# Performance work log

Measured on AMD Instinct MI355X. Metric: run time of the kernel, lower is better.

## Reference

```python
import jax, jax.numpy as jnp
import numpy as np
import math

D_MODEL, N_HEADS, D_K, D_V = 512, 2, 64, 64
C_CLIP = 10.0
MASK_FILL = -10.0

def setup_inputs() -> dict:
    key = jax.random.key(0)
    ks = jax.random.split(key, 12)
    B, Lq, Lk = 4, 2048, 2048
    s = 1.0 / math.sqrt(D_MODEL)
    return {
        "Q": jax.random.normal(ks[0], (B, Lq, D_MODEL), jnp.float32),
        "K": jax.random.normal(ks[1], (B, Lk, D_MODEL), jnp.float32),
        "V": jax.random.normal(ks[2], (B, Lk, D_MODEL), jnp.float32),
        "mask": jax.random.randint(ks[3], (B, Lk), 0, 2) > 0,
        "Wq": jax.random.normal(ks[4], (D_MODEL, N_HEADS * D_K), jnp.float32) * s,
        "bq": jnp.zeros((N_HEADS * D_K,), jnp.float32),
        "Wk": jax.random.normal(ks[5], (D_MODEL, N_HEADS * D_K), jnp.float32) * s,
        "bk": jnp.zeros((N_HEADS * D_K,), jnp.float32),
        "Wv": jax.random.normal(ks[6], (D_MODEL, N_HEADS * D_V), jnp.float32) * s,
        "bv": jnp.zeros((N_HEADS * D_V,), jnp.float32),
        "Wo": jax.random.normal(ks[7], (N_HEADS * D_V, D_MODEL), jnp.float32) * s,
        "bo": jnp.zeros((D_MODEL,), jnp.float32),
    }

def reference(Q, K, V, mask, Wq, bq, Wk, bk, Wv, bv, Wo, bo):
    B, Lq, _ = Q.shape
    Lk = K.shape[1]
    # project and split heads: [B, h, L, d]
    q = (Q @ Wq + bq).reshape(B, Lq, N_HEADS, D_K).transpose(0, 2, 1, 3)
    k = (K @ Wk + bk).reshape(B, Lk, N_HEADS, D_K).transpose(0, 2, 1, 3)
    v = (V @ Wv + bv).reshape(B, Lk, N_HEADS, D_V).transpose(0, 2, 1, 3)
    scores = jnp.einsum("bhqd,bhkd->bhqk", q, k) / jnp.sqrt(jnp.float32(D_K))
    scores = jnp.tanh(scores) * C_CLIP
    scores = jnp.where(mask[:, None, None, :], MASK_FILL, scores)
    attn = jax.nn.log_softmax(scores, axis=-1)  # NOTE: log-softmax used directly as weights
    out = jnp.einsum("bhqk,bhkd->bhqd", attn, v)
    out = out.transpose(0, 2, 1, 3).reshape(B, Lq, N_HEADS * D_V)
    out = out @ Wo + bo
    return (out, attn)
```

## Files before the change

### kernel.cpp

```cpp
#include <hip/hip_runtime.h>

typedef __attribute__((ext_vector_type(8))) short short8;
typedef __attribute__((ext_vector_type(4))) short short4v;
typedef __attribute__((ext_vector_type(4))) float f32x4;

#define DEVI static __device__ __forceinline__

constexpr int NB   = 4;
constexpr int NH   = 2;
constexpr int SEQ  = 2048;
constexpr int DM   = 512;
constexpr int DKV  = 64;
constexpr int HDIM = 128;

DEVI unsigned short f2bf(float f) {
    union { float f; unsigned u; } v; v.f = f;
    unsigned r = v.u + 0x7FFFu + ((v.u >> 16) & 1u);
    return (unsigned short)(r >> 16);
}
DEVI float bf2f(unsigned short s) {
    union { unsigned u; float f; } v; v.u = ((unsigned)s) << 16; return v.f;
}
DEVI void async16(const void* g, void* l) {
    __builtin_amdgcn_global_load_lds(
        (const __attribute__((address_space(1))) unsigned int*)g,
        (__attribute__((address_space(3))) unsigned int*)l, 16, 0, 0);
}

__global__ __launch_bounds__(256) void k_prep(
    const float* __restrict__ Wq, const float* __restrict__ Wk,
    const float* __restrict__ Wv, const float* __restrict__ Wo,
    unsigned short* __restrict__ Wqt, unsigned short* __restrict__ Wkt,
    unsigned short* __restrict__ Wvt, unsigned short* __restrict__ Wot) {
    int id = blockIdx.x * 256 + threadIdx.x;
    int which = id >> 16;
    int rem = id & 65535;
    if (which < 3) {
        const float* W = which == 0 ? Wq : (which == 1 ? Wk : Wv);
        unsigned short* Wt = which == 0 ? Wqt : (which == 1 ? Wkt : Wvt);
        int n = rem >> 9, k = rem & 511;
        Wt[rem] = f2bf(W[k * HDIM + n]);
    } else {
        int n = rem >> 7, k = rem & 127;
        Wot[rem] = f2bf(Wo[k * DM + n]);
    }
}

__global__ __launch_bounds__(256) void k_proj(
    const float* __restrict__ Qg, const float* __restrict__ Kg, const float* __restrict__ Vg,
    const unsigned short* __restrict__ Wqt, const unsigned short* __restrict__ Wkt,
    const unsigned short* __restrict__ Wvt,
    const float* __restrict__ bq, const float* __restrict__ bk, const float* __restrict__ bv,
    unsigned short* __restrict__ qs, unsigned short* __restrict__ kb,
    unsigned short* __restrict__ vt) {
    __shared__ unsigned short lA[64 * 64];
    __shared__ unsigned short lB[128 * 64];

    const int y = blockIdx.y;
    const float* X = y == 0 ? Qg : (y == 1 ? Kg : Vg);
    const unsigned short* Wt = y == 0 ? Wqt : (y == 1 ? Wkt : Wvt);
    const float* bias = y == 0 ? bq : (y == 1 ? bk : bv);
    const float scal = y == 0 ? 0.125f : 1.0f;
    const int row0 = blockIdx.x * 64;
    const int tid = threadIdx.x, lane = tid & 63, wv = tid >> 6;
    const int l16 = lane & 15, lq4 = lane >> 4;
    const int wr = wv >> 1, wc = wv & 1;

    f32x4 acc[2][4];
    #pragma unroll
    for (int i = 0; i < 2; ++i)
        #pragma unroll
        for (int j = 0; j < 4; ++j) acc[i][j] = f32x4{0.f, 0.f, 0.f, 0.f};

    const int arow = tid >> 2, ac0 = (tid & 3) * 16;

    for (int kc = 0; kc < 8; ++kc) {
        {
            const float* src = X + (size_t)(row0 + arow) * DM + kc * 64 + ac0;
            unsigned short* dst = &lA[arow * 64 + ac0];
            #pragma unroll
            for (int i = 0; i < 4; ++i) {
                float4 v = *(const float4*)(src + 4 * i);
                unsigned p0 = (unsigned)f2bf(v.x) | ((unsigned)f2bf(v.y) << 16);
                unsigned p1 = (unsigned)f2bf(v.z) | ((unsigned)f2bf(v.w) << 16);
                *(unsigned*)(dst + 4 * i) = p0;
                *(unsigned*)(dst + 4 * i + 2) = p1;
            }
        }
        #pragma unroll
        for (int c = 0; c < 4; ++c) {
            int chunk = wv * 4 + c;
            int n = chunk * 8 + (lane >> 3);
            int kpart = (lane & 7) * 8;
            const void* g = (const char*)Wt + ((size_t)n * DM + kc * 64 + kpart) * 2;
            void* l = (char*)lB + chunk * 1024 + lane * 16;
            async16(g, l);
        }
        __syncthreads();

        #pragma unroll
        for (int ks = 0; ks < 2; ++ks) {
            short8 a[2], b[4];
            #pragma unroll
            for (int mt = 0; mt < 2; ++mt) {
                int m = wr * 32 + mt * 16 + l16;
                a[mt] = *(const short8*)&lA[m * 64 + ks * 32 + lq4 * 8];
            }
            #pragma unroll
            for (int nt = 0; nt < 4; ++nt) {
                int n = wc * 64 + nt * 16 + l16;
                b[nt] = *(const short8*)&lB[n * 64 + ks * 32 + lq4 * 8];
            }
            #pragma unroll
            for (int mt = 0; mt < 2; ++mt)
                #pragma unroll
                for (int nt = 0; nt < 4; ++nt)
                    acc[mt][nt] = __builtin_amdgcn_mfma_f32_16x16x32_bf16(
                        a[mt], b[nt], acc[mt][nt], 0, 0, 0);
        }
        __syncthreads();
    }

    if (y < 2) {
        unsigned short* dstp = (y == 0) ? qs : kb;
        #pragma unroll
        for (int mt = 0; mt < 2; ++mt)
            #pragma unroll
            for (int nt = 0; nt < 4; ++nt) {
                int col = wc * 64 + nt * 16 + l16;
                float bb = bias[col];
                int h = col >> 6, d = col & 63;
                #pragma unroll
                for (int r = 0; r < 4; ++r) {
                    int row = row0 + wr * 32 + mt * 16 + lq4 * 4 + r;
                    int b = row >> 11, pos = row & 2047;
                    float val = (acc[mt][nt][r] + bb) * scal;
                    dstp[((size_t)(b * NH + h) * SEQ + pos) * DKV + d] = f2bf(val);
                }
            }
    } else {
        #pragma unroll
        for (int mt = 0; mt < 2; ++mt)
            #pragma unroll
            for (int nt = 0; nt < 4; ++nt) {
                int col = wc * 64 + nt * 16 + l16;
                float bb = bias[col];
                #pragma unroll
                for (int r = 0; r < 4; ++r) {
                    int mrow = wr * 32 + mt * 16 + lq4 * 4 + r;
                    lB[col * 64 + mrow] = f2bf(acc[mt][nt][r] + bb);
                }
            }
        __syncthreads();
        int c = tid >> 1, mp = (tid & 1) * 32;
        int b = row0 >> 11, kpos0 = row0 & 2047;
        int h = c >> 6, d = c & 63;
        unsigned short* dst = vt + ((size_t)(b * NH + h) * DKV + d) * SEQ + kpos0 + mp;
        const unsigned short* srcl = &lB[c * 64 + mp];
        #pragma unroll
        for (int i = 0; i < 4; ++i)
            *(uint4*)(dst + 8 * i) = *(const uint4*)(srcl + 8 * i);
    }
}

__global__ __launch_bounds__(256) void k_pass1(
    const unsigned short* __restrict__ qs, const unsigned short* __restrict__ kb,
    const int* __restrict__ maskg, float* __restrict__ Lpart) {
    __shared__ unsigned short lK[128 * 64];
    __shared__ int lM[128];
    __shared__ float lsumW[4 * 64];

    const int bx = blockIdx.x;
    const int ksp = bx & 3;
    const int qt = (bx >> 2) & 31;
    const int bh = bx >> 7;
    const int qbase = qt * 64;
    const int b = bh >> 1;
    const int tid = threadIdx.x, lane = tid & 63, wv = tid >> 6;
    const int l16 = lane & 15, lq4 = lane >> 4;

    short8 aq[4][2];
    #pragma unroll
    for (int mt = 0; mt < 4; ++mt)
        #pragma unroll
        for (int ks = 0; ks < 2; ++ks) {
            size_t off = ((size_t)bh * SEQ + qbase + mt * 16 + l16) * DKV + ks * 32 + lq4 * 8;
            aq[mt][ks] = *(const short8*)(qs + off);
        }

    float sums[4][4];
    #pragma unroll
    for (int mt = 0; mt < 4; ++mt)
        #pragma unroll
        for (int r = 0; r < 4; ++r) sums[mt][r] = 0.f;

    const char* kbase_ptr = (const char*)(kb + (size_t)bh * SEQ * DKV);

    for (int kt = ksp * 4; kt < ksp * 4 + 4; ++kt) {
        int kbase = kt * 128;
        #pragma unroll
        for (int c = 0; c < 4; ++c) {
            int chunk = wv * 4 + c;
            const void* g = kbase_ptr + (size_t)kbase * 128 + chunk * 1024 + lane * 16;
            void* l = (char*)lK + chunk * 1024 + lane * 16;
            async16(g, l);
        }
        if (tid < 128) lM[tid] = maskg[b * SEQ + kbase + tid];
        __syncthreads();

        f32x4 acc[4][2];
        #pragma unroll
        for (int mt = 0; mt < 4; ++mt)
            #pragma unroll
            for (int nt = 0; nt < 2; ++nt) acc[mt][nt] = f32x4{0.f, 0.f, 0.f, 0.f};
        #pragma unroll
        for (int ks = 0; ks < 2; ++ks) {
            short8 bfr[2];
            #pragma unroll
            for (int nt = 0; nt < 2; ++nt) {
                int n = wv * 32 + nt * 16 + l16;
                bfr[nt] = *(const short8*)&lK[n * 64 + ks * 32 + lq4 * 8];
            }
            #pragma unroll
            for (int mt = 0; mt < 4; ++mt)
                #pragma unroll
                for (int nt = 0; nt < 2; ++nt)
                    acc[mt][nt] = __builtin_amdgcn_mfma_f32_16x16x32_bf16(
                        aq[mt][ks], bfr[nt], acc[mt][nt], 0, 0, 0);
        }
        #pragma unroll
        for (int nt = 0; nt < 2; ++nt) {
            int col = wv * 32 + nt * 16 + l16;
            int mv = lM[col];
            #pragma unroll
            for (int mt = 0; mt < 4; ++mt)
                #pragma unroll
                for (int r = 0; r < 4; ++r) {
                    float x = acc[mt][nt][r];
                    float e2 = __expf(2.f * x);
                    float s10 = 10.f - 20.f * __builtin_amdgcn_rcpf(1.f + e2);
                    float s = mv ? -10.f : s10;
                    sums[mt][r] += __expf(s);
                }
        }
        __syncthreads();
    }

    #pragma unroll
    for (int mt = 0; mt < 4; ++mt)
        #pragma unroll
        for (int r = 0; r < 4; ++r) {
            float v = sums[mt][r];
            v += __shfl_xor(v, 1); v += __shfl_xor(v, 2);
            v += __shfl_xor(v, 4); v += __shfl_xor(v, 8);
            if (l16 == 0) lsumW[wv * 64 + mt * 16 + lq4 * 4 + r] = v;
        }
    __syncthreads();
    if (tid < 64) {
        float v = lsumW[tid] + lsumW[64 + tid] + lsumW[128 + tid] + lsumW[192 + tid];
        Lpart[(size_t)ksp * (8 * SEQ) + (size_t)bh * SEQ + qbase + tid] = v;
    }
}

__global__ __launch_bounds__(256) void k_pass2(
    const unsigned short* __restrict__ qs, const unsigned short* __restrict__ kb,
    const unsigned short* __restrict__ vt, const int* __restrict__ maskg,
    const float* __restrict__ Lpart, float* __restrict__ attnG, float* __restrict__ outh2) {
    __shared__ unsigned short lK[128 * 64];
    __shared__ unsigned short lV[64 * 128];
    __shared__ unsigned short lAttn[64 * 136];
    __shared__ int lM[128];

    const int bx = blockIdx.x;
    const int ksp = bx & 3;
    const int qt = (bx >> 2) & 31;
    const int bh = bx >> 7;
    const int qbase = qt * 64;
    const int b = bh >> 1, h = bh & 1;
    const int tid = threadIdx.x, lane = tid & 63, wv = tid >> 6;
    const int l16 = lane & 15, lq4 = lane >> 4;

    short8 aq[4][2];
    #pragma unroll
    for (int mt = 0; mt < 4; ++mt)
        #pragma unroll
        for (int ks = 0; ks < 2; ++ks) {
            size_t off = ((size_t)bh * SEQ + qbase + mt * 16 + l16) * DKV + ks * 32 + lq4 * 8;
            aq[mt][ks] = *(const short8*)(qs + off);
        }

    float Lr[4][4];
    #pragma unroll
    for (int mt = 0; mt < 4; ++mt)
        #pragma unroll
        for (int r = 0; r < 4; ++r) {
            size_t idx = (size_t)bh * SEQ + qbase + mt * 16 + lq4 * 4 + r;
            float s = Lpart[idx] + Lpart[8 * SEQ + idx] +
                      Lpart[2 * 8 * SEQ + idx] + Lpart[3 * 8 * SEQ + idx];
            Lr[mt][r] = __logf(s);
        }

    f32x4 o[4];
    #pragma unroll
    for (int mt = 0; mt < 4; ++mt) o[mt] = f32x4{0.f, 0.f, 0.f, 0.f};

    const char* kbase_ptr = (const char*)(kb + (size_t)bh * SEQ * DKV);

    for (int kt = ksp * 4; kt < ksp * 4 + 4; ++kt) {
        int kbase = kt * 128;
        #pragma unroll
        for (int c = 0; c < 4; ++c) {
            int chunk = wv * 4 + c;
            const void* g = kbase_ptr + (size_t)kbase * 128 + chunk * 1024 + lane * 16;
            void* l = (char*)lK + chunk * 1024 + lane * 16;
            async16(g, l);
        }
        #pragma unroll
        for (int c = 0; c < 4; ++c) {
            int chunk = wv * 4 + c;
            int d = chunk * 4 + (lane >> 4);
            int kk = (lane & 15) * 8;
            const void* g = (const char*)vt + (((size_t)bh * DKV + d) * SEQ + kbase + kk) * 2;
            void* l = (char*)lV + chunk * 1024 + lane * 16;
            async16(g, l);
        }
        if (tid < 128) lM[tid] = maskg[b * SEQ + kbase + tid];
        __syncthreads();

        f32x4 s[4][2];
        #pragma unroll
        for (int mt = 0; mt < 4; ++mt)
            #pragma unroll
            for (int nt = 0; nt < 2; ++nt) s[mt][nt] = f32x4{0.f, 0.f, 0.f, 0.f};
        #pragma unroll
        for (int ks = 0; ks < 2; ++ks) {
            short8 bfr[2];
            #pragma unroll
            for (int nt = 0; nt < 2; ++nt) {
                int n = wv * 32 + nt * 16 + l16;
                bfr[nt] = *(const short8*)&lK[n * 64 + ks * 32 + lq4 * 8];
            }
            #pragma unroll
            for (int mt = 0; mt < 4; ++mt)
                #pragma unroll
                for (int nt = 0; nt < 2; ++nt)
                    s[mt][nt] = __builtin_amdgcn_mfma_f32_16x16x32_bf16(
                        aq[mt][ks], bfr[nt], s[mt][nt], 0, 0, 0);
        }
        #pragma unroll
        for (int nt = 0; nt < 2; ++nt) {
            int col = wv * 32 + nt * 16 + l16;
            int mv = lM[col];
            #pragma unroll
            for (int mt = 0; mt < 4; ++mt)
                #pragma unroll
                for (int r = 0; r < 4; ++r) {
                    float x = s[mt][nt][r];
                    float e2 = __expf(2.f * x);
                    float s10 = 10.f - 20.f * __builtin_amdgcn_rcpf(1.f + e2);
                    float a = (mv ? -10.f : s10) - Lr[mt][r];
                    lAttn[(mt * 16 + lq4 * 4 + r) * 136 + col] = f2bf(a);
                }
        }
        __syncthreads();

        #pragma unroll
        for (int ks = 0; ks < 4; ++ks) {
            short8 bfr = *(const short8*)&lV[(wv * 16 + l16) * 128 + ks * 32 + lq4 * 8];
            #pragma unroll
            for (int mt = 0; mt < 4; ++mt) {
                short8 af = *(const short8*)&lAttn[(mt * 16 + l16) * 136 + ks * 32 + lq4 * 8];
                o[mt] = __builtin_amdgcn_mfma_f32_16x16x32_bf16(af, bfr, o[mt], 0, 0, 0);
            }
        }
        #pragma unroll
        for (int j = 0; j < 8; ++j) {
            int row = j * 8 + (tid >> 5);
            int col = (tid & 31) * 4;
            short4v hv = *(const short4v*)&lAttn[row * 136 + col];
            float4 f;
            f.x = bf2f((unsigned short)hv[0]); f.y = bf2f((unsigned short)hv[1]);
            f.z = bf2f((unsigned short)hv[2]); f.w = bf2f((unsigned short)hv[3]);
            float* gdst = attnG + ((size_t)bh * SEQ + qbase + row) * SEQ + kbase + col;
            *(float4*)gdst = f;
        }
        __syncthreads();
    }

    float* dst = outh2 + (size_t)ksp * (8192 * HDIM);
    #pragma unroll
    for (int mt = 0; mt < 4; ++mt)
        #pragma unroll
        for (int r = 0; r < 4; ++r) {
            int q = qbase + mt * 16 + lq4 * 4 + r;
            int dcol = wv * 16 + l16;
            dst[((size_t)b * SEQ + q) * HDIM + h * DKV + dcol] = o[mt][r];
        }
}

__global__ __launch_bounds__(256) void k_comb(const float* __restrict__ outh2,
                                              unsigned short* __restrict__ outh) {
    int i = (blockIdx.x * 256 + threadIdx.x) * 4;
    float4 a = *(const float4*)(outh2 + i);
    float4 c = *(const float4*)(outh2 + 1048576 + i);
    float4 d = *(const float4*)(outh2 + 2 * 1048576 + i);
    float4 e = *(const float4*)(outh2 + 3 * 1048576 + i);
    unsigned long long pk =
        (unsigned long long)f2bf(a.x + c.x + d.x + e.x) |
        ((unsigned long long)f2bf(a.y + c.y + d.y + e.y) << 16) |
        ((unsigned long long)f2bf(a.z + c.z + d.z + e.z) << 32) |
        ((unsigned long long)f2bf(a.w + c.w + d.w + e.w) << 48);
    *(unsigned long long*)(outh + i) = pk;
}

__global__ __launch_bounds__(256) void k_oproj(
    const unsigned short* __restrict__ outh, const unsigned short* __restrict__ Wot,
    const float* __restrict__ bo, float* __restrict__ outG) {
    __shared__ unsigned short lA2[128 * 128];
    __shared__ unsigned short lB2[128 * 128];
    const int row0 = blockIdx.x * 128, col0 = blockIdx.y * 128;
    const int tid = threadIdx.x, lane = tid & 63, wv = tid >> 6;
    const int l16 = lane & 15, lq4 = lane >> 4;
    const int wr = wv >> 1, wc = wv & 1;

    #pragma unroll
    for (int c = 0; c < 8; ++c) {
        int chunk = wv * 8 + c;
        const void* g = (const char*)outh + (size_t)row0 * 256 + chunk * 1024 + lane * 16;
        void* l = (char*)lA2 + chunk * 1024 + lane * 16;
        async16(g, l);
    }
    #pragma unroll
    for (int c = 0; c < 8; ++c) {
        int chunk = wv * 8 + c;
        const void* g = (const char*)Wot + (size_t)col0 * 256 + chunk * 1024 + lane * 16;
        void* l = (char*)lB2 + chunk * 1024 + lane * 16;
        async16(g, l);
    }
    __syncthreads();

    f32x4 acc[4][4];
    #pragma unroll
    for (int mt = 0; mt < 4; ++mt)
        #pragma unroll
        for (int nt = 0; nt < 4; ++nt) acc[mt][nt] = f32x4{0.f, 0.f, 0.f, 0.f};

    #pragma unroll
    for (int ks = 0; ks < 4; ++ks) {
        short8 a[4], bfr[4];
        #pragma unroll
        for (int mt = 0; mt < 4; ++mt)
            a[mt] = *(const short8*)&lA2[(wr * 64 + mt * 16 + l16) * 128 + ks * 32 + lq4 * 8];
        #pragma unroll
        for (int nt = 0; nt < 4; ++nt)
            bfr[nt] = *(const short8*)&lB2[(wc * 64 + nt * 16 + l16) * 128 + ks * 32 + lq4 * 8];
        #pragma unroll
        for (int mt = 0; mt < 4; ++mt)
            #pragma unroll
            for (int nt = 0; nt < 4; ++nt)
                acc[mt][nt] = __builtin_amdgcn_mfma_f32_16x16x32_bf16(
                    a[mt], bfr[nt], acc[mt][nt], 0, 0, 0);
    }

    #pragma unroll
    for (int nt = 0; nt < 4; ++nt) {
        int col = col0 + wc * 64 + nt * 16 + l16;
        float bb = bo[col];
        #pragma unroll
        for (int mt = 0; mt < 4; ++mt)
            #pragma unroll
            for (int r = 0; r < 4; ++r) {
                int row = row0 + wr * 64 + mt * 16 + lq4 * 4 + r;
                outG[(size_t)row * DM + col] = acc[mt][nt][r] + bb;
            }
    }
}

extern "C" void kernel_launch(void* const* d_in, const int* in_sizes, int n_in,
                              void* d_out, int out_size, void* d_ws, size_t ws_size,
                              hipStream_t stream) {
    (void)in_sizes; (void)n_in; (void)out_size; (void)ws_size;
    const float* Qg = (const float*)d_in[0];
    const float* Kg = (const float*)d_in[1];
    const float* Vg = (const float*)d_in[2];
    const int*   maskg = (const int*)d_in[3];
    const float* Wq = (const float*)d_in[4];
    const float* bq = (const float*)d_in[5];
    const float* Wk = (const float*)d_in[6];
    const float* bk = (const float*)d_in[7];
    const float* Wv = (const float*)d_in[8];
    const float* bv = (const float*)d_in[9];
    const float* Wo = (const float*)d_in[10];
    const float* bo = (const float*)d_in[11];

    char* ws = (char*)d_ws;
    unsigned short* qs   = (unsigned short*)(ws);
    unsigned short* kb   = (unsigned short*)(ws + (4  << 20));
    unsigned short* vt   = (unsigned short*)(ws + (8  << 20));
    float*          outh2= (float*)(ws + (12 << 20));
    unsigned short* outh = (unsigned short*)(ws + (28 << 20));
    float*          Lpart= (float*)(ws + (30 << 20));
    unsigned short* Wqt  = (unsigned short*)(ws + (30 << 20) + 262144);
    unsigned short* Wkt  = (unsigned short*)((char*)Wqt + 131072);
    unsigned short* Wvt  = (unsigned short*)((char*)Wkt + 131072);
    unsigned short* Wot  = (unsigned short*)((char*)Wvt + 131072);

    float* outG  = (float*)d_out;
    float* attnG = outG + (size_t)NB * SEQ * DM;

    hipLaunchKernelGGL(k_prep, dim3(1024), dim3(256), 0, stream,
                       Wq, Wk, Wv, Wo, Wqt, Wkt, Wvt, Wot);
    hipLaunchKernelGGL(k_proj, dim3(128, 3), dim3(256), 0, stream,
                       Qg, Kg, Vg, Wqt, Wkt, Wvt, bq, bk, bv, qs, kb, vt);
    hipLaunchKernelGGL(k_pass1, dim3(1024), dim3(256), 0, stream, qs, kb, maskg, Lpart);
    hipLaunchKernelGGL(k_pass2, dim3(1024), dim3(256), 0, stream,
                       qs, kb, vt, maskg, Lpart, attnG, outh2);
    hipLaunchKernelGGL(k_comb, dim3(1024), dim3(256), 0, stream, outh2, outh);
    hipLaunchKernelGGL(k_oproj, dim3(64, 4), dim3(256), 0, stream, outh, Wot, bo, outG);
}
```

Baseline: 261.7 us.

## Store clipped scores in pass1, factor log-sum out of PV, fuse combine

Pass1 now writes the bf16 tanh-clipped scores to a 64MB workspace, so pass2 no longer recomputes QK^T. Pass2 multiplies the raw scores by V and subtracts L times the per-column sum of V, which k_proj accumulates with atomics. Pass2 also reads the stored scores to write the attention output with nontemporal stores. The combine kernel is folded into the output projection, and several shared-memory tiles get XOR swizzles or padding against bank conflicts. The cost is an extra write and read of the full score matrix through global memory, plus a small precision change from factoring out the log-sum.

```diff
diff --git a/kernel.cpp b/kernel.cpp
--- a/kernel.cpp
+++ b/kernel.cpp
@@ -1,7 +1,6 @@
 #include <hip/hip_runtime.h>
 
 typedef __attribute__((ext_vector_type(8))) short short8;
-typedef __attribute__((ext_vector_type(4))) short short4v;
 typedef __attribute__((ext_vector_type(4))) float f32x4;
 
 #define DEVI static __device__ __forceinline__
@@ -52,8 +51,8 @@
     const unsigned short* __restrict__ Wvt,
     const float* __restrict__ bq, const float* __restrict__ bk, const float* __restrict__ bv,
     unsigned short* __restrict__ qs, unsigned short* __restrict__ kb,
-    unsigned short* __restrict__ vt) {
-    __shared__ unsigned short lA[64 * 64];
+    unsigned short* __restrict__ vt, float* __restrict__ colsumv) {
+    __shared__ unsigned short lA[64 * 72];
     __shared__ unsigned short lB[128 * 64];
 
     const int y = blockIdx.y;
@@ -77,10 +76,10 @@
     for (int kc = 0; kc < 8; ++kc) {
         {
             const float* src = X + (size_t)(row0 + arow) * DM + kc * 64 + ac0;
-            unsigned short* dst = &lA[arow * 64 + ac0];
+            unsigned short* dst = &lA[arow * 72 + ac0];
             #pragma unroll
             for (int i = 0; i < 4; ++i) {
-                float4 v = *(const float4*)(src + 4 * i);
+                f32x4 v = __builtin_nontemporal_load((const f32x4*)(src + 4 * i));
                 unsigned p0 = (unsigned)f2bf(v.x) | ((unsigned)f2bf(v.y) << 16);
                 unsigned p1 = (unsigned)f2bf(v.z) | ((unsigned)f2bf(v.w) << 16);
                 *(unsigned*)(dst + 4 * i) = p0;
@@ -90,9 +89,9 @@
         #pragma unroll
         for (int c = 0; c < 4; ++c) {
             int chunk = wv * 4 + c;
-            int n = chunk * 8 + (lane >> 3);
-            int kpart = (lane & 7) * 8;
-            const void* g = (const char*)Wt + ((size_t)n * DM + kc * 64 + kpart) * 2;
+            int flat = chunk * 64 + lane;
+            int row = flat >> 3, cp = flat & 7, cc = cp ^ (row & 7);
+            const void* g = (const char*)Wt + (size_t)row * 1024 + kc * 128 + cc * 16;
             void* l = (char*)lB + chunk * 1024 + lane * 16;
             async16(g, l);
         }
@@ -104,12 +103,12 @@
             #pragma unroll
             for (int mt = 0; mt < 2; ++mt) {
                 int m = wr * 32 + mt * 16 + l16;
-                a[mt] = *(const short8*)&lA[m * 64 + ks * 32 + lq4 * 8];
+                a[mt] = *(const short8*)&lA[m * 72 + ks * 32 + lq4 * 8];
             }
             #pragma unroll
             for (int nt = 0; nt < 4; ++nt) {
                 int n = wc * 64 + nt * 16 + l16;
-                b[nt] = *(const short8*)&lB[n * 64 + ks * 32 + lq4 * 8];
+                b[nt] = *(const short8*)&lB[n * 64 + (((ks * 4 + lq4) ^ (n & 7)) * 8)];
             }
             #pragma unroll
             for (int mt = 0; mt < 2; ++mt)
@@ -152,21 +151,41 @@
                 }
             }
         __syncthreads();
-        int c = tid >> 1, mp = (tid & 1) * 32;
-        int b = row0 >> 11, kpos0 = row0 & 2047;
-        int h = c >> 6, d = c & 63;
-        unsigned short* dst = vt + ((size_t)(b * NH + h) * DKV + d) * SEQ + kpos0 + mp;
-        const unsigned short* srcl = &lB[c * 64 + mp];
-        #pragma unroll
-        for (int i = 0; i < 4; ++i)
-            *(uint4*)(dst + 8 * i) = *(const uint4*)(srcl + 8 * i);
+        {
+            int c = tid >> 1, mp = (tid & 1) * 32;
+            int b = row0 >> 11, kpos0 = row0 & 2047;
+            int h = c >> 6, d = c & 63;
+            unsigned short* dst = vt + ((size_t)(b * NH + h) * DKV + d) * SEQ + kpos0 + mp;
+            const unsigned short* srcl = &lB[c * 64 + mp];
+            #pragma unroll
+            for (int i = 0; i < 4; ++i)
+                *(uint4*)(dst + 8 * i) = *(const uint4*)(srcl + 8 * i);
+        }
+        {
+            int col = tid >> 1, half = tid & 1;
+            const unsigned short* p = &lB[col * 64 + half * 32];
+            float s = 0.f;
+            #pragma unroll
+            for (int i = 0; i < 4; ++i) {
+                short8 hv = *(const short8*)(p + 8 * i);
+                #pragma unroll
+                for (int j = 0; j < 8; ++j) s += bf2f((unsigned short)hv[j]);
+            }
+            s += __shfl_xor(s, 1);
+            if (half == 0) {
+                int ksp2 = (row0 & 2047) >> 9, bb = row0 >> 11;
+                atomicAdd(&colsumv[((size_t)ksp2 * NB + bb) * HDIM + col], s);
+            }
+        }
     }
 }
 
 __global__ __launch_bounds__(256) void k_pass1(
     const unsigned short* __restrict__ qs, const unsigned short* __restrict__ kb,
-    const int* __restrict__ maskg, float* __restrict__ Lpart) {
+    const int* __restrict__ maskg, unsigned short* __restrict__ sws,
+    float* __restrict__ Lpart) {
     __shared__ unsigned short lK[128 * 64];
+    __shared__ unsigned short lS[64 * 136];
     __shared__ int lM[128];
     __shared__ float lsumW[4 * 64];
 
@@ -201,7 +220,9 @@
         #pragma unroll
         for (int c = 0; c < 4; ++c) {
             int chunk = wv * 4 + c;
-            const void* g = kbase_ptr + (size_t)kbase * 128 + chunk * 1024 + lane * 16;
+            int flat = chunk * 64 + lane;
+            int row = flat >> 3, cp = flat & 7, cc = cp ^ (row & 7);
+            const void* g = kbase_ptr + (size_t)(kbase + row) * 128 + cc * 16;
             void* l = (char*)lK + chunk * 1024 + lane * 16;
             async16(g, l);
         }
@@ -219,7 +240,7 @@
             #pragma unroll
             for (int nt = 0; nt < 2; ++nt) {
                 int n = wv * 32 + nt * 16 + l16;
-                bfr[nt] = *(const short8*)&lK[n * 64 + ks * 32 + lq4 * 8];
+                bfr[nt] = *(const short8*)&lK[n * 64 + (((ks * 4 + lq4) ^ (n & 7)) * 8)];
             }
             #pragma unroll
             for (int mt = 0; mt < 4; ++mt)
@@ -238,12 +259,23 @@
                 for (int r = 0; r < 4; ++r) {
                     float x = acc[mt][nt][r];
                     float e2 = __expf(2.f * x);
-                    float s10 = 10.f - 20.f * __builtin_amdgcn_rcpf(1.f + e2);
-                    float s = mv ? -10.f : s10;
-                    sums[mt][r] += __expf(s);
+                    float rr = __builtin_amdgcn_rcpf(1.f + e2);
+                    rr = mv ? 1.f : rr;
+                    float s10 = __builtin_fmaf(-20.f, rr, 10.f);
+                    union { float f; unsigned u; } cv; cv.f = s10;
+                    lS[(mt * 16 + lq4 * 4 + r) * 136 + col] = (unsigned short)(cv.u >> 16);
+                    float t = __expf(-20.f * rr);
+                    sums[mt][r] = __builtin_fmaf(22026.465795f, t, sums[mt][r]);
                 }
         }
         __syncthreads();
+        #pragma unroll
+        for (int j = 0; j < 4; ++j) {
+            int row = j * 16 + (tid >> 4);
+            int coff = (tid & 15) * 8;
+            uint4 dv = *(const uint4*)&lS[row * 136 + coff];
+            *(uint4*)(sws + ((size_t)bh * SEQ + qbase + row) * SEQ + kbase + coff) = dv;
+        }
     }
 
     #pragma unroll
@@ -263,13 +295,11 @@
 }
 
 __global__ __launch_bounds__(256) void k_pass2(
-    const unsigned short* __restrict__ qs, const unsigned short* __restrict__ kb,
-    const unsigned short* __restrict__ vt, const int* __restrict__ maskg,
-    const float* __restrict__ Lpart, float* __restrict__ attnG, float* __restrict__ outh2) {
-    __shared__ unsigned short lK[128 * 64];
+    const unsigned short* __restrict__ sws, const unsigned short* __restrict__ vt,
+    const float* __restrict__ Lpart, const float* __restrict__ colsumv,
+    float* __restrict__ attnG, float* __restrict__ outh2) {
     __shared__ unsigned short lV[64 * 128];
-    __shared__ unsigned short lAttn[64 * 136];
-    __shared__ int lM[128];
+    __shared__ float lL[64];
 
     const int bx = blockIdx.x;
     const int ksp = bx & 3;
@@ -280,141 +310,84 @@
     const int tid = threadIdx.x, lane = tid & 63, wv = tid >> 6;
     const int l16 = lane & 15, lq4 = lane >> 4;
 
-    short8 aq[4][2];
+    if (tid < 64) {
+        size_t idx = (size_t)bh * SEQ + qbase + tid;
+        float s = Lpart[idx] + Lpart[8 * SEQ + idx] +
+                  Lpart[2 * 8 * SEQ + idx] + Lpart[3 * 8 * SEQ + idx];
+        lL[tid] = __logf(s);
+    }
+    __syncthreads();
+
+    float Lr[4][4];
     #pragma unroll
     for (int mt = 0; mt < 4; ++mt)
         #pragma unroll
-        for (int ks = 0; ks < 2; ++ks) {
-            size_t off = ((size_t)bh * SEQ + qbase + mt * 16 + l16) * DKV + ks * 32 + lq4 * 8;
-            aq[mt][ks] = *(const short8*)(qs + off);
-        }
-
-    float Lr[4][4];
-    #pragma unroll
-    for (int mt = 0; mt < 4; ++mt)
-        #pragma unroll
-        for (int r = 0; r < 4; ++r) {
-            size_t idx = (size_t)bh * SEQ + qbase + mt * 16 + lq4 * 4 + r;
-            float s = Lpart[idx] + Lpart[8 * SEQ + idx] +
-                      Lpart[2 * 8 * SEQ + idx] + Lpart[3 * 8 * SEQ + idx];
-            Lr[mt][r] = __logf(s);
-        }
+        for (int r = 0; r < 4; ++r) Lr[mt][r] = lL[mt * 16 + lq4 * 4 + r];
 
     f32x4 o[4];
     #pragma unroll
     for (int mt = 0; mt < 4; ++mt) o[mt] = f32x4{0.f, 0.f, 0.f, 0.f};
 
-    const char* kbase_ptr = (const char*)(kb + (size_t)bh * SEQ * DKV);
-
-    for (int kt = ksp * 4; kt < ksp * 4 + 4; ++kt) {
-        int kbase = kt * 128;
+    const unsigned short* swsb = sws + (size_t)bh * SEQ * SEQ;
+
+    for (int kti = 0; kti < 4; ++kti) {
+        int kbase = ksp * 512 + kti * 128;
         #pragma unroll
         for (int c = 0; c < 4; ++c) {
             int chunk = wv * 4 + c;
-            const void* g = kbase_ptr + (size_t)kbase * 128 + chunk * 1024 + lane * 16;
-            void* l = (char*)lK + chunk * 1024 + lane * 16;
-            async16(g, l);
-        }
-        #pragma unroll
-        for (int c = 0; c < 4; ++c) {
-            int chunk = wv * 4 + c;
-            int d = chunk * 4 + (lane >> 4);
-            int kk = (lane & 15) * 8;
-            const void* g = (const char*)vt + (((size_t)bh * DKV + d) * SEQ + kbase + kk) * 2;
+            int flat = chunk * 64 + lane;
+            int row = flat >> 4, cp = flat & 15, cc = cp ^ (row & 15);
+            const void* g = (const char*)vt +
+                (((size_t)bh * DKV + row) * SEQ + kbase) * 2 + cc * 16;
             void* l = (char*)lV + chunk * 1024 + lane * 16;
             async16(g, l);
         }
-        if (tid < 128) lM[tid] = maskg[b * SEQ + kbase + tid];
-        __syncthreads();
-
-        f32x4 s[4][2];
-        #pragma unroll
-        for (int mt = 0; mt < 4; ++mt)
-            #pragma unroll
-            for (int nt = 0; nt < 2; ++nt) s[mt][nt] = f32x4{0.f, 0.f, 0.f, 0.f};
-        #pragma unroll
-        for (int ks = 0; ks < 2; ++ks) {
-            short8 bfr[2];
-            #pragma unroll
-            for (int nt = 0; nt < 2; ++nt) {
-                int n = wv * 32 + nt * 16 + l16;
-                bfr[nt] = *(const short8*)&lK[n * 64 + ks * 32 + lq4 * 8];
-            }
-            #pragma unroll
-            for (int mt = 0; mt < 4; ++mt)
-                #pragma unroll
-                for (int nt = 0; nt < 2; ++nt)
-                    s[mt][nt] = __builtin_amdgcn_mfma_f32_16x16x32_bf16(
-                        aq[mt][ks], bfr[nt], s[mt][nt], 0, 0, 0);
-        }
-        #pragma unroll
-        for (int nt = 0; nt < 2; ++nt) {
-            int col = wv * 32 + nt * 16 + l16;
-            int mv = lM[col];
-            #pragma unroll
-            for (int mt = 0; mt < 4; ++mt)
-                #pragma unroll
-                for (int r = 0; r < 4; ++r) {
-                    float x = s[mt][nt][r];
-                    float e2 = __expf(2.f * x);
-                    float s10 = 10.f - 20.f * __builtin_amdgcn_rcpf(1.f + e2);
-                    float a = (mv ? -10.f : s10) - Lr[mt][r];
-                    lAttn[(mt * 16 + lq4 * 4 + r) * 136 + col] = f2bf(a);
-                }
-        }
         __syncthreads();
 
         #pragma unroll
         for (int ks = 0; ks < 4; ++ks) {
-            short8 bfr = *(const short8*)&lV[(wv * 16 + l16) * 128 + ks * 32 + lq4 * 8];
+            int d = wv * 16 + l16;
+            short8 bfr = *(const short8*)&lV[d * 128 + (((ks * 4 + lq4) ^ (d & 15)) * 8)];
             #pragma unroll
             for (int mt = 0; mt < 4; ++mt) {
-                short8 af = *(const short8*)&lAttn[(mt * 16 + l16) * 136 + ks * 32 + lq4 * 8];
+                const unsigned short* ap = swsb +
+                    (size_t)(qbase + mt * 16 + l16) * SEQ + kbase + ks * 32 + lq4 * 8;
+                short8 af = *(const short8*)ap;
                 o[mt] = __builtin_amdgcn_mfma_f32_16x16x32_bf16(af, bfr, o[mt], 0, 0, 0);
             }
         }
-        #pragma unroll
-        for (int j = 0; j < 8; ++j) {
-            int row = j * 8 + (tid >> 5);
-            int col = (tid & 31) * 4;
-            short4v hv = *(const short4v*)&lAttn[row * 136 + col];
-            float4 f;
-            f.x = bf2f((unsigned short)hv[0]); f.y = bf2f((unsigned short)hv[1]);
-            f.z = bf2f((unsigned short)hv[2]); f.w = bf2f((unsigned short)hv[3]);
-            float* gdst = attnG + ((size_t)bh * SEQ + qbase + row) * SEQ + kbase + col;
-            *(float4*)gdst = f;
-        }
-        __syncthreads();
-    }
-
+
+        #pragma unroll
+        for (int jr = 0; jr < 8; ++jr) {
+            int row = jr * 8 + (tid >> 5);
+            float Lv = lL[row];
+            size_t roff = (size_t)(qbase + row) * SEQ + kbase + (tid & 31) * 4;
+            uint2 w = *(const uint2*)(swsb + roff);
+            union { unsigned u; float f; } t0, t1, t2, t3;
+            t0.u = w.x << 16; t1.u = w.x & 0xFFFF0000u;
+            t2.u = w.y << 16; t3.u = w.y & 0xFFFF0000u;
+            f32x4 f;
+            f.x = t0.f - Lv; f.y = t1.f - Lv; f.z = t2.f - Lv; f.w = t3.f - Lv;
+            __builtin_nontemporal_store(f, (f32x4*)(attnG + (size_t)bh * SEQ * SEQ + roff));
+        }
+        __syncthreads();
+    }
+
+    int dcol = wv * 16 + l16;
+    float csv = colsumv[((size_t)ksp * NB + b) * HDIM + h * DKV + dcol];
     float* dst = outh2 + (size_t)ksp * (8192 * HDIM);
     #pragma unroll
     for (int mt = 0; mt < 4; ++mt)
         #pragma unroll
         for (int r = 0; r < 4; ++r) {
             int q = qbase + mt * 16 + lq4 * 4 + r;
-            int dcol = wv * 16 + l16;
-            dst[((size_t)b * SEQ + q) * HDIM + h * DKV + dcol] = o[mt][r];
-        }
-}
-
-__global__ __launch_bounds__(256) void k_comb(const float* __restrict__ outh2,
-                                              unsigned short* __restrict__ outh) {
-    int i = (blockIdx.x * 256 + threadIdx.x) * 4;
-    float4 a = *(const float4*)(outh2 + i);
-    float4 c = *(const float4*)(outh2 + 1048576 + i);
-    float4 d = *(const float4*)(outh2 + 2 * 1048576 + i);
-    float4 e = *(const float4*)(outh2 + 3 * 1048576 + i);
-    unsigned long long pk =
-        (unsigned long long)f2bf(a.x + c.x + d.x + e.x) |
-        ((unsigned long long)f2bf(a.y + c.y + d.y + e.y) << 16) |
-        ((unsigned long long)f2bf(a.z + c.z + d.z + e.z) << 32) |
-        ((unsigned long long)f2bf(a.w + c.w + d.w + e.w) << 48);
-    *(unsigned long long*)(outh + i) = pk;
+            float val = o[mt][r] - Lr[mt][r] * csv;
+            dst[((size_t)b * SEQ + q) * HDIM + h * DKV + dcol] = val;
+        }
 }
 
 __global__ __launch_bounds__(256) void k_oproj(
-    const unsigned short* __restrict__ outh, const unsigned short* __restrict__ Wot,
+    const float* __restrict__ outh2, const unsigned short* __restrict__ Wot,
     const float* __restrict__ bo, float* __restrict__ outG) {
     __shared__ unsigned short lA2[128 * 128];
     __shared__ unsigned short lB2[128 * 128];
@@ -424,16 +397,33 @@
     const int wr = wv >> 1, wc = wv & 1;
 
     #pragma unroll
+    for (int jj = 0; jj < 8; ++jj) {
+        int flat = jj * 256 + tid;
+        int row = flat >> 4, c = flat & 15;
+        size_t gr = (size_t)(row0 + row) * HDIM + c * 8;
+        float s[8];
+        #pragma unroll
+        for (int i = 0; i < 8; ++i) s[i] = 0.f;
+        #pragma unroll
+        for (int qq = 0; qq < 4; ++qq) {
+            const float4* p = (const float4*)(outh2 + (size_t)qq * 1048576 + gr);
+            float4 x0 = p[0], x1 = p[1];
+            s[0] += x0.x; s[1] += x0.y; s[2] += x0.z; s[3] += x0.w;
+            s[4] += x1.x; s[5] += x1.y; s[6] += x1.z; s[7] += x1.w;
+        }
+        unsigned d0 = (unsigned)f2bf(s[0]) | ((unsigned)f2bf(s[1]) << 16);
+        unsigned d1 = (unsigned)f2bf(s[2]) | ((unsigned)f2bf(s[3]) << 16);
+        unsigned d2 = (unsigned)f2bf(s[4]) | ((unsigned)f2bf(s[5]) << 16);
+        unsigned d3 = (unsigned)f2bf(s[6]) | ((unsigned)f2bf(s[7]) << 16);
+        uint4 pk; pk.x = d0; pk.y = d1; pk.z = d2; pk.w = d3;
+        *(uint4*)&lA2[row * 128 + ((c ^ (row & 15)) * 8)] = pk;
+    }
+    #pragma unroll
     for (int c = 0; c < 8; ++c) {
         int chunk = wv * 8 + c;
-        const void* g = (const char*)outh + (size_t)row0 * 256 + chunk * 1024 + lane * 16;
-        void* l = (char*)lA2 + chunk * 1024 + lane * 16;
-        async16(g, l);
-    }
-    #pragma unroll
-    for (int c = 0; c < 8; ++c) {
-        int chunk = wv * 8 + c;
-        const void* g = (const char*)Wot + (size_t)col0 * 256 + chunk * 1024 + lane * 16;
+        int flat = chunk * 64 + lane;
+        int row = flat >> 4, cp = flat & 15, cc = cp ^ (row & 15);
+        const void* g = (const char*)Wot + ((size_t)(col0 + row) * 128 + cc * 8) * 2;
         void* l = (char*)lB2 + chunk * 1024 + lane * 16;
         async16(g, l);
     }
@@ -449,11 +439,15 @@
     for (int ks = 0; ks < 4; ++ks) {
         short8 a[4], bfr[4];
         #pragma unroll
-        for (int mt = 0; mt < 4; ++mt)
-            a[mt] = *(const short8*)&lA2[(wr * 64 + mt * 16 + l16) * 128 + ks * 32 + lq4 * 8];
-        #pragma unroll
-        for (int nt = 0; nt < 4; ++nt)
-            bfr[nt] = *(const short8*)&lB2[(wc * 64 + nt * 16 + l16) * 128 + ks * 32 + lq4 * 8];
+        for (int mt = 0; mt < 4; ++mt) {
+            int row = wr * 64 + mt * 16 + l16;
+            a[mt] = *(const short8*)&lA2[row * 128 + (((ks * 4 + lq4) ^ (row & 15)) * 8)];
+        }
+        #pragma unroll
+        for (int nt = 0; nt < 4; ++nt) {
+            int row = wc * 64 + nt * 16 + l16;
+            bfr[nt] = *(const short8*)&lB2[row * 128 + (((ks * 4 + lq4) ^ (row & 15)) * 8)];
+        }
         #pragma unroll
         for (int mt = 0; mt < 4; ++mt)
             #pragma unroll
@@ -494,27 +488,30 @@
     const float* bo = (const float*)d_in[11];
 
     char* ws = (char*)d_ws;
-    unsigned short* qs   = (unsigned short*)(ws);
-    unsigned short* kb   = (unsigned short*)(ws + (4  << 20));
-    unsigned short* vt   = (unsigned short*)(ws + (8  << 20));
-    float*          outh2= (float*)(ws + (12 << 20));
-    unsigned short* outh = (unsigned short*)(ws + (28 << 20));
-    float*          Lpart= (float*)(ws + (30 << 20));
-    unsigned short* Wqt  = (unsigned short*)(ws + (30 << 20) + 262144);
-    unsigned short* Wkt  = (unsigned short*)((char*)Wqt + 131072);
-    unsigned short* Wvt  = (unsigned short*)((char*)Wkt + 131072);
-    unsigned short* Wot  = (unsigned short*)((char*)Wvt + 131072);
+    unsigned short* qs    = (unsigned short*)(ws);
+    unsigned short* kb    = (unsigned short*)(ws + (4  << 20));
+    unsigned short* vt    = (unsigned short*)(ws + (8  << 20));
+    unsigned short* sws   = (unsigned short*)(ws + (12 << 20));
+    float*          outh2 = (float*)(ws + (76 << 20));
+    float*          Lpart = (float*)(ws + (92 << 20));
+    float*          colsumv = (float*)(ws + (92 << 20) + 262144);
+    unsigned short* Wqt   = (unsigned short*)(ws + (92 << 20) + 524288);
+    unsigned short* Wkt   = (unsigned short*)((char*)Wqt + 131072);
+    unsigned short* Wvt   = (unsigned short*)((char*)Wkt + 131072);
+    unsigned short* Wot   = (unsigned short*)((char*)Wvt + 131072);
 
     float* outG  = (float*)d_out;
     float* attnG = outG + (size_t)NB * SEQ * DM;
 
+    (void)hipMemsetAsync(colsumv, 0, 16 * HDIM * sizeof(float), stream);
     hipLaunchKernelGGL(k_prep, dim3(1024), dim3(256), 0, stream,
                        Wq, Wk, Wv, Wo, Wqt, Wkt, Wvt, Wot);
     hipLaunchKernelGGL(k_proj, dim3(128, 3), dim3(256), 0, stream,
-                       Qg, Kg, Vg, Wqt, Wkt, Wvt, bq, bk, bv, qs, kb, vt);
-    hipLaunchKernelGGL(k_pass1, dim3(1024), dim3(256), 0, stream, qs, kb, maskg, Lpart);
+                       Qg, Kg, Vg, Wqt, Wkt, Wvt, bq, bk, bv, qs, kb, vt, colsumv);
+    hipLaunchKernelGGL(k_pass1, dim3(1024), dim3(256), 0, stream,
+                       qs, kb, maskg, sws, Lpart);
     hipLaunchKernelGGL(k_pass2, dim3(1024), dim3(256), 0, stream,
-                       qs, kb, vt, maskg, Lpart, attnG, outh2);
-    hipLaunchKernelGGL(k_comb, dim3(1024), dim3(256), 0, stream, outh2, outh);
-    hipLaunchKernelGGL(k_oproj, dim3(64, 4), dim3(256), 0, stream, outh, Wot, bo, outG);
-}
+                       sws, vt, Lpart, colsumv, attnG, outh2);
+    hipLaunchKernelGGL(k_oproj, dim3(64, 4), dim3(256), 0, stream,
+                       outh2, Wot, bo, outG);
+}
```

Result: slower. 289.0 us (+10.4%).
